# Optimization experiments

Measured on AMD Instinct MI355X. Metric: run time of the kernel, lower is better.

The kernel has to match this reference:

```python
import jax, jax.numpy as jnp
import numpy as np

# ---- model / batching constants (DeepSeek-LLM-7B attention, chunked prefill) ----
B = 8            # sequences in the continuous batch
Q_LEN = 512      # new (query) tokens per sequence
HIST = 512       # history tokens already in cache
NH = 32          # query heads
NKV = 32         # kv heads (== NH for deepseek 7B)
HD = 128         # head dim
HIDDEN = NH * HD # 4096
BS = 64          # paged-cache block size
NBLK = 16        # blocks per sequence -> kv_len = 1024
KV_LEN = BS * NBLK
NUM_BLOCKS = B * NBLK
ROPE_BASE = 10000.0


def rotate_half(x):
    x1, x2 = jnp.split(x, 2, axis=-1)
    return jnp.concatenate([-x2, x1], axis=-1)


def setup_inputs() -> dict:
    key = jax.random.key(0)
    ks = jax.random.split(key, 8)
    T = B * Q_LEN
    hidden_states = jax.random.normal(ks[0], (T, HIDDEN), jnp.float32)
    Wq = jax.random.normal(ks[1], (HIDDEN, NH * HD), jnp.float32) * 0.02
    Wk = jax.random.normal(ks[2], (HIDDEN, NKV * HD), jnp.float32) * 0.02
    Wv = jax.random.normal(ks[3], (HIDDEN, NKV * HD), jnp.float32) * 0.02
    Wo = jax.random.normal(ks[4], (NH * HD, HIDDEN), jnp.float32) * 0.02
    # paged KV cache; first HIST positions of each sequence hold history K/V
    k_cache = jax.random.normal(ks[5], (NUM_BLOCKS, BS, NKV, HD), jnp.float32) * 0.5
    v_cache = jax.random.normal(ks[6], (NUM_BLOCKS, BS, NKV, HD), jnp.float32) * 0.5
    # block table: each sequence gets NBLK distinct physical blocks (permuted)
    block_offsets = jnp.asarray(
        np.random.default_rng(0).permutation(NUM_BLOCKS).reshape(B, NBLK),
        jnp.int32)
    # per-token absolute position within its sequence (history offset + local idx)
    position_ids_1d = (jnp.arange(T, dtype=jnp.int32) % Q_LEN) + HIST
    kv_seq_length = jnp.full((B,), HIST + Q_LEN, jnp.int32)
    return dict(hidden_states=hidden_states, Wq=Wq, Wk=Wk, Wv=Wv, Wo=Wo,
                k_cache=k_cache, v_cache=v_cache, block_offsets=block_offsets,
                position_ids_1d=position_ids_1d, kv_seq_length=kv_seq_length)


def reference(hidden_states, Wq, Wk, Wv, Wo, k_cache, v_cache,
              block_offsets, position_ids_1d, kv_seq_length):
    T = hidden_states.shape[0]
    # --- QKV projections ---
    q = (hidden_states @ Wq).reshape(T, NH, HD)
    k = (hidden_states @ Wk).reshape(T, NKV, HD)
    v = (hidden_states @ Wv).reshape(T, NKV, HD)
    # --- RoPE (per-token positions, continuous batching) ---
    inv_freq = 1.0 / (ROPE_BASE ** (jnp.arange(0, HD, 2, dtype=jnp.float32) / HD))
    freqs = position_ids_1d.astype(jnp.float32)[:, None] * inv_freq  # [T, HD/2]
    emb = jnp.concatenate([freqs, freqs], axis=-1)                    # [T, HD]
    cos = jnp.cos(emb)[:, None, :]
    sin = jnp.sin(emb)[:, None, :]
    q = q * cos + rotate_half(q) * sin
    k = k * cos + rotate_half(k) * sin
    # --- fill_kv_cache: scatter new K/V into paged cache via block table ---
    seq_idx = jnp.arange(T, dtype=jnp.int32) // Q_LEN
    blk = block_offsets[seq_idx, position_ids_1d // BS]  # [T] physical block id
    slot = position_ids_1d % BS                          # [T] slot within block
    k_cache = k_cache.at[blk, slot].set(k)
    v_cache = v_cache.at[blk, slot].set(v)
    # --- paged_attention_fwd: gather per-seq K/V via block table ---
    K = k_cache[block_offsets].reshape(B, KV_LEN, NKV, HD)
    V = v_cache[block_offsets].reshape(B, KV_LEN, NKV, HD)
    qb = q.reshape(B, Q_LEN, NH, HD)
    scale = 1.0 / jnp.sqrt(jnp.float32(HD))
    scores = jnp.einsum('bqhd,bkhd->bhqk', qb, K) * scale  # [B,NH,Q,KV]
    kv_pos = jnp.arange(KV_LEN, dtype=jnp.int32)
    q_pos = position_ids_1d.reshape(B, Q_LEN)
    mask = (kv_pos[None, None, :] <= q_pos[:, :, None]) & \
           (kv_pos[None, None, :] < kv_seq_length[:, None, None])  # [B,Q,KV]
    scores = jnp.where(mask[:, None, :, :], scores, jnp.finfo(scores.dtype).min)
    attn = jax.nn.softmax(scores, axis=-1)
    out = jnp.einsum('bhqk,bkhd->bqhd', attn, V).reshape(T, NH * HD)
    return out @ Wo
```

## Files before the change

kernel.cpp:

```cpp
#include <hip/hip_runtime.h>
#include <math.h>

typedef __bf16 bf16x8 __attribute__((ext_vector_type(8)));
typedef float floatx4 __attribute__((ext_vector_type(4)));
typedef unsigned short ushortx4 __attribute__((ext_vector_type(4)));
typedef unsigned short ushortx8 __attribute__((ext_vector_type(8)));

#define DEV __device__ __forceinline__

DEV unsigned short f2bf(float f){
  unsigned int u = __float_as_uint(f);
  return (unsigned short)((u + 0x7fffu + ((u >> 16) & 1u)) >> 16);
}
DEV float bf2f(unsigned short h){ return __uint_as_float(((unsigned int)h) << 16); }

DEV void gld16(const void* g, void* l){
  __builtin_amdgcn_global_load_lds((const __attribute__((address_space(1))) void*)g,
                                   (__attribute__((address_space(3))) void*)l, 16, 0, 0);
}
DEV floatx4 mfma16(bf16x8 a, bf16x8 b, floatx4 c){
  return __builtin_amdgcn_mfma_f32_16x16x32_bf16(a, b, c, 0, 0, 0);
}

#define NH 32
#define HD 128
#define QL 512
#define KVL 1024
#define HID 4096

__global__ void k_convert(const float* __restrict__ src, unsigned short* __restrict__ dst){
  size_t u = (size_t)blockIdx.x*256 + threadIdx.x;
  float4 a = ((const float4*)src)[2*u];
  float4 b = ((const float4*)src)[2*u+1];
  ushortx8 o;
  o[0]=f2bf(a.x); o[1]=f2bf(a.y); o[2]=f2bf(a.z); o[3]=f2bf(a.w);
  o[4]=f2bf(b.x); o[5]=f2bf(b.y); o[6]=f2bf(b.z); o[7]=f2bf(b.w);
  ((ushortx8*)dst)[u] = o;
}

__global__ void k_transpose_w(const float* __restrict__ W0, const float* __restrict__ W1,
                              const float* __restrict__ W2, const float* __restrict__ W3,
                              unsigned short* __restrict__ Wt){
  int bx = blockIdx.x, by = blockIdx.y, z = blockIdx.z;
  const float* src = (z==0)?W0:(z==1)?W1:(z==2)?W2:W3;
  __shared__ float t[64][65];
  int tid = threadIdx.x;
  int rr = tid >> 4, cc = tid & 15;
  #pragma unroll
  for (int p = 0; p < 4; ++p){
    int row = p*16 + rr;
    float4 v = *(const float4*)(src + (size_t)(by*64+row)*HID + bx*64 + cc*4);
    t[row][cc*4+0]=v.x; t[row][cc*4+1]=v.y; t[row][cc*4+2]=v.z; t[row][cc*4+3]=v.w;
  }
  __syncthreads();
  unsigned short* dst = Wt + (size_t)z*HID*HID;
  #pragma unroll
  for (int p = 0; p < 4; ++p){
    int orow = p*16 + rr;
    ushortx4 o;
    o[0]=f2bf(t[cc*4+0][orow]); o[1]=f2bf(t[cc*4+1][orow]);
    o[2]=f2bf(t[cc*4+2][orow]); o[3]=f2bf(t[cc*4+3][orow]);
    *(ushortx4*)(dst + (size_t)(bx*64+orow)*HID + by*64 + cc*4) = o;
  }
}

template<int MODE>
__global__ __launch_bounds__(256, 4) void k_gemm(
    const unsigned short* __restrict__ A, const unsigned short* __restrict__ Bt,
    float* __restrict__ Cf, unsigned short* __restrict__ Qr,
    unsigned short* __restrict__ Kf, unsigned short* __restrict__ Vtmp,
    int K, int N, int Ntiles)
{
  __shared__ __align__(16) unsigned short As[128*32];
  __shared__ __align__(16) unsigned short Bs[128*32];
  const int tid = threadIdx.x;
  const int wave = tid >> 6, lane = tid & 63;
  const int lm = lane & 15, quad = lane >> 4;
  const int wm = wave >> 1, wn = wave & 1;

  int lin = blockIdx.x;
  int xcd = lin & 7, loc = lin >> 3;
  int per = Ntiles * 2;
  int phase = loc / per, rr2 = loc - phase*per;
  const int bm = xcd*4 + phase*2 + (rr2 & 1);
  const int bn = rr2 >> 1;

  const char* gA[2]; const char* gB[2];
  unsigned short* lA[2]; unsigned short* lB[2];
  #pragma unroll
  for (int jj = 0; jj < 2; ++jj){
    int issue = wave*2 + jj;
    int row = issue*16 + (lane >> 2);
    int c = (lane & 3) ^ ((row >> 1) & 3);
    gA[jj] = (const char*)(A + (size_t)(bm*128 + row)*K) + c*16;
    gB[jj] = (const char*)(Bt + (size_t)(bn*128 + row)*K) + c*16;
    lA[jj] = As + issue*512;
    lB[jj] = Bs + issue*512;
  }
  floatx4 acc[4][4];
  #pragma unroll
  for (int i=0;i<4;i++)
    #pragma unroll
    for (int j=0;j<4;j++) acc[i][j] = (floatx4){0.f,0.f,0.f,0.f};

  int aoff[4], boff[4];
  #pragma unroll
  for (int i=0;i<4;i++){
    int rowA = wm*64 + i*16 + lm;
    aoff[i] = rowA*32 + (quad ^ ((rowA>>1)&3))*8;
    int rowB = wn*64 + i*16 + lm;
    boff[i] = rowB*32 + (quad ^ ((rowB>>1)&3))*8;
  }

  const int kIter = K >> 5;
  for (int kt = 0; kt < kIter; ++kt){
    #pragma unroll
    for (int jj=0;jj<2;jj++){ gld16(gA[jj], lA[jj]); gld16(gB[jj], lB[jj]); }
    __syncthreads();
    bf16x8 af[4], bfr[4];
    #pragma unroll
    for (int i=0;i<4;i++) af[i]  = *(const bf16x8*)(As + aoff[i]);
    #pragma unroll
    for (int i=0;i<4;i++) bfr[i] = *(const bf16x8*)(Bs + boff[i]);
    #pragma unroll
    for (int mi=0;mi<4;mi++)
      #pragma unroll
      for (int ni=0;ni<4;ni++)
        acc[mi][ni] = mfma16(af[mi], bfr[ni], acc[mi][ni]);
    __syncthreads();
    #pragma unroll
    for (int jj=0;jj<2;jj++){ gA[jj] += 64; gB[jj] += 64; }
  }

  #pragma unroll
  for (int mi=0;mi<4;mi++){
    #pragma unroll
    for (int ni=0;ni<4;ni++){
      #pragma unroll
      for (int r=0;r<4;r++){
        int trow = bm*128 + wm*64 + mi*16 + quad*4 + r;
        int col  = bn*128 + wn*64 + ni*16 + lm;
        float val = acc[mi][ni][r];
        if (MODE == 0){
          Cf[(size_t)trow*N + col] = val;
        } else {
          unsigned short bv = f2bf(val);
          int b = trow >> 9, qi = trow & 511;
          if (col < 4096){
            int hh = col >> 7, hd = col & 127;
            Qr[((size_t)(b*NH + hh)*QL + qi)*HD + hd] = bv;
          } else if (col < 8192){
            int cc2 = col - 4096; int hh = cc2 >> 7, hd = cc2 & 127;
            Kf[((size_t)(b*NH + hh)*KVL + 512 + qi)*HD + hd] = bv;
          } else {
            Vtmp[(size_t)trow*HID + (col - 8192)] = bv;
          }
        }
      }
    }
  }
}

__global__ void k_rope(unsigned short* __restrict__ Qr, unsigned short* __restrict__ Kf,
                       const int* __restrict__ pos_ids){
  int u = blockIdx.x*256 + threadIdx.x;
  int i = u & 63;
  int grp = u >> 6;
  int qi = grp & 511;
  int h = (grp >> 9) & 31;
  int b = grp >> 14;
  int t = b*QL + qi;
  int pos = pos_ids[t];
  float ang = (float)pos * exp2f((float)i * -0.20762050593046014f);
  float s, c;
  sincosf(ang, &s, &c);
  unsigned short* qp = Qr + ((size_t)(b*NH + h)*QL + qi)*HD;
  float x = bf2f(qp[i]), y = bf2f(qp[i+64]);
  qp[i]    = f2bf(x*c - y*s);
  qp[i+64] = f2bf(y*c + x*s);
  unsigned short* kp = Kf + ((size_t)(b*NH + h)*KVL + 512 + qi)*HD;
  x = bf2f(kp[i]); y = bf2f(kp[i+64]);
  kp[i]    = f2bf(x*c - y*s);
  kp[i+64] = f2bf(y*c + x*s);
}

__global__ void k_gather_k(const float* __restrict__ k_cache, const int* __restrict__ block_offsets,
                           unsigned short* __restrict__ Kf){
  int u = blockIdx.x*256 + threadIdx.x;
  int c4 = u & 31;
  int h  = (u >> 5) & 31;
  int kv = (u >> 10) & 511;
  int b  = u >> 19;
  int blk = block_offsets[b*16 + (kv >> 6)];
  int slot = kv & 63;
  float4 v = *(const float4*)(k_cache + ((size_t)(blk*64 + slot)*NH + h)*HD + c4*4);
  ushortx4 o; o[0]=f2bf(v.x); o[1]=f2bf(v.y); o[2]=f2bf(v.z); o[3]=f2bf(v.w);
  *(ushortx4*)(Kf + ((size_t)(b*NH + h)*KVL + kv)*HD + c4*4) = o;
}

__global__ void k_transpose_v(const float* __restrict__ v_cache, const unsigned short* __restrict__ Vtmp,
                              const int* __restrict__ block_offsets, unsigned short* __restrict__ Vt){
  int kvt = blockIdx.x, h = blockIdx.y, b = blockIdx.z;
  __shared__ __align__(16) unsigned short tt[64*132];
  int tid = threadIdx.x;
  #pragma unroll
  for (int p=0;p<8;p++){
    int cc = p*256 + tid;
    int slot = cc >> 5, c4 = cc & 31;
    ushortx4 val;
    if (kvt < 8){
      int blk = block_offsets[b*16 + kvt];
      float4 f = *(const float4*)(v_cache + ((size_t)(blk*64 + slot)*NH + h)*HD + c4*4);
      val[0]=f2bf(f.x); val[1]=f2bf(f.y); val[2]=f2bf(f.z); val[3]=f2bf(f.w);
    } else {
      val = *(const ushortx4*)(Vtmp + (size_t)(b*QL + (kvt-8)*64 + slot)*HID + h*HD + c4*4);
    }
    *(ushortx4*)(tt + slot*132 + c4*4) = val;
  }
  __syncthreads();
  #pragma unroll
  for (int p=0;p<8;p++){
    int cc = p*256 + tid;
    int hd = cc >> 4, s4 = cc & 15;
    ushortx4 o;
    o[0]=tt[(s4*4+0)*132 + hd];
    o[1]=tt[(s4*4+1)*132 + hd];
    o[2]=tt[(s4*4+2)*132 + hd];
    o[3]=tt[(s4*4+3)*132 + hd];
    *(ushortx4*)(Vt + ((size_t)(b*NH + h)*HD + hd)*KVL + kvt*64 + s4*4) = o;
  }
}

DEV void stage128(const char* srcBase, unsigned short* lds, int rowStrideBytes, int wave, int lane){
  #pragma unroll
  for (int jj=0;jj<8;jj++){
    int issue = wave*8 + jj;
    int row = issue*4 + (lane >> 4);
    int c = (lane & 15) ^ (row & 15);
    gld16(srcBase + (size_t)row*rowStrideBytes + c*16, lds + issue*512);
  }
}
DEV bf16x8 frag_swz(const unsigned short* lds, int row, int ks, int quad){
  int c = (ks*4 + quad) ^ (row & 15);
  return *(const bf16x8*)(lds + row*128 + c*8);
}

#define PSTR 144

__global__ __launch_bounds__(256, 1) void k_attn(
    const unsigned short* __restrict__ Qr, const unsigned short* __restrict__ Kf,
    const unsigned short* __restrict__ Vt, unsigned short* __restrict__ AO)
{
  int qt = blockIdx.x, h = blockIdx.y, b = blockIdx.z;
  int tid = threadIdx.x, wave = tid >> 6, lane = tid & 63;
  int lm = lane & 15, quad = lane >> 4;
  __shared__ __align__(16) unsigned short KS[2][128*128];
  __shared__ __align__(16) unsigned short VS[128*128];
  __shared__ __align__(16) unsigned short PS[4*32*PSTR];
  const char* Qbase = (const char*)(Qr + ((size_t)(b*NH + h)*QL + qt*128)*HD);
  const char* Kbase = (const char*)(Kf + ((size_t)(b*NH + h)*KVL)*HD);
  const char* Vbase = (const char*)(Vt + ((size_t)(b*NH + h)*HD)*KVL);

  stage128(Qbase, VS, 256, wave, lane);
  stage128(Kbase, KS[0], 256, wave, lane);
  __syncthreads();
  bf16x8 qf[2][4];
  #pragma unroll
  for (int mt=0;mt<2;mt++)
    #pragma unroll
    for (int ks=0;ks<4;ks++)
      qf[mt][ks] = frag_swz(VS, wave*32 + mt*16 + lm, ks, quad);
  __syncthreads();

  float m_st[2][4], l_st[2][4];
  floatx4 o[2][8];
  #pragma unroll
  for (int mt=0;mt<2;mt++){
    #pragma unroll
    for (int r=0;r<4;r++){ m_st[mt][r] = -3.0e38f; l_st[mt][r] = 0.f; }
    #pragma unroll
    for (int nt=0;nt<8;nt++) o[mt][nt] = (floatx4){0.f,0.f,0.f,0.f};
  }
  unsigned short* myP = PS + wave*(32*PSTR);
  const int sig = ((lm & 3) << 2) | (lm >> 2);
  const float scale = 0.08838834764831845f;
  int ntiles = qt + 5;

  for (int j=0;j<ntiles;j++){
    const unsigned short* cur = KS[j & 1];
    unsigned short* nxt = (unsigned short*)KS[(j+1) & 1];
    stage128(Vbase + (size_t)j*256, VS, 2048, wave, lane);
    if (j+1 < ntiles) stage128(Kbase + (size_t)(j+1)*128*256, nxt, 256, wave, lane);

    floatx4 s[2][8];
    #pragma unroll
    for (int nt=0;nt<8;nt++){
      bf16x8 kf4[4];
      #pragma unroll
      for (int ks=0;ks<4;ks++) kf4[ks] = frag_swz(cur, nt*16 + lm, ks, quad);
      #pragma unroll
      for (int mt=0;mt<2;mt++){
        floatx4 a = (floatx4){0.f,0.f,0.f,0.f};
        #pragma unroll
        for (int ks=0;ks<4;ks++) a = mfma16(qf[mt][ks], kf4[ks], a);
        s[mt][nt] = a;
      }
    }
    bool diag = (j == qt + 4);
    #pragma unroll
    for (int mt=0;mt<2;mt++){
      #pragma unroll
      for (int r=0;r<4;r++){
        int rowl = wave*32 + mt*16 + quad*4 + r;
        float mx = -3.0e38f;
        #pragma unroll
        for (int nt=0;nt<8;nt++){
          float v = s[mt][nt][r] * scale;
          if (diag && (nt*16 + lm > rowl)) v = -3.0e38f;
          s[mt][nt][r] = v;
          mx = fmaxf(mx, v);
        }
        mx = fmaxf(mx, __shfl_xor(mx, 1));
        mx = fmaxf(mx, __shfl_xor(mx, 2));
        mx = fmaxf(mx, __shfl_xor(mx, 4));
        mx = fmaxf(mx, __shfl_xor(mx, 8));
        float mold = m_st[mt][r];
        float mnew = fmaxf(mold, mx);
        float alpha = __expf(mold - mnew);
        m_st[mt][r] = mnew;
        float rs = 0.f;
        #pragma unroll
        for (int nt=0;nt<8;nt++){
          float p = __expf(s[mt][nt][r] - mnew);
          s[mt][nt][r] = p;
          rs += p;
        }
        rs += __shfl_xor(rs, 1);
        rs += __shfl_xor(rs, 2);
        rs += __shfl_xor(rs, 4);
        rs += __shfl_xor(rs, 8);
        l_st[mt][r] = l_st[mt][r]*alpha + rs;
        #pragma unroll
        for (int nt=0;nt<8;nt++) o[mt][nt][r] *= alpha;
      }
    }
    #pragma unroll
    for (int mt=0;mt<2;mt++)
      #pragma unroll
      for (int nt=0;nt<8;nt++)
        #pragma unroll
        for (int r=0;r<4;r++)
          myP[(mt*16 + r*4 + quad)*PSTR + nt*16 + lm] = f2bf(s[mt][nt][r]);

    __syncthreads();

    bf16x8 pf[2][4];
    #pragma unroll
    for (int mt=0;mt<2;mt++)
      #pragma unroll
      for (int ks=0;ks<4;ks++)
        pf[mt][ks] = *(const bf16x8*)(myP + (mt*16 + sig)*PSTR + ks*32 + quad*8);

    #pragma unroll
    for (int nt=0;nt<8;nt++){
      bf16x8 vf4[4];
      #pragma unroll
      for (int ks=0;ks<4;ks++) vf4[ks] = frag_swz(VS, nt*16 + lm, ks, quad);
      #pragma unroll
      for (int mt=0;mt<2;mt++){
        floatx4 a = o[mt][nt];
        #pragma unroll
        for (int ks=0;ks<4;ks++) a = mfma16(pf[mt][ks], vf4[ks], a);
        o[mt][nt] = a;
      }
    }
    __syncthreads();
  }

  #pragma unroll
  for (int mt=0;mt<2;mt++){
    #pragma unroll
    for (int r=0;r<4;r++){
      float inv = 1.f / l_st[mt][r];
      #pragma unroll
      for (int nt=0;nt<8;nt++){
        int trow = b*QL + qt*128 + wave*32 + mt*16 + quad*4 + r;
        int col = h*HD + nt*16 + lm;
        AO[(size_t)trow*HID + col] = f2bf(o[mt][nt][r] * inv);
      }
    }
  }
}

extern "C" void kernel_launch(void* const* d_in, const int* in_sizes, int n_in,
                              void* d_out, int out_size, void* d_ws, size_t ws_size,
                              hipStream_t stream) {
  const float* hidden   = (const float*)d_in[0];
  const float* Wq       = (const float*)d_in[1];
  const float* Wk       = (const float*)d_in[2];
  const float* Wv       = (const float*)d_in[3];
  const float* Wo       = (const float*)d_in[4];
  const float* k_cache  = (const float*)d_in[5];
  const float* v_cache  = (const float*)d_in[6];
  const int* block_offsets = (const int*)d_in[7];
  const int* pos_ids    = (const int*)d_in[8];
  float* out = (float*)d_out;

  char* ws = (char*)d_ws;
  unsigned short* hb   = (unsigned short*)(ws + 0x0);
  unsigned short* Wt   = (unsigned short*)(ws + 0x2000000);
  unsigned short* Qr   = (unsigned short*)(ws + 0xA000000);
  unsigned short* Kf   = (unsigned short*)(ws + 0xC000000);
  unsigned short* Vt   = (unsigned short*)(ws + 0x10000000);
  unsigned short* Vtmp = (unsigned short*)(ws + 0x14000000);
  unsigned short* AO   = hb;

  k_convert<<<8192, 256, 0, stream>>>(hidden, hb);
  k_transpose_w<<<dim3(64,64,4), 256, 0, stream>>>(Wq, Wk, Wv, Wo, Wt);
  k_gemm<1><<<3072, 256, 0, stream>>>(hb, Wt, nullptr, Qr, Kf, Vtmp, 4096, 12288, 96);
  k_rope<<<32768, 256, 0, stream>>>(Qr, Kf, pos_ids);
  k_gather_k<<<16384, 256, 0, stream>>>(k_cache, block_offsets, Kf);
  k_transpose_v<<<dim3(16,32,8), 256, 0, stream>>>(v_cache, Vtmp, block_offsets, Vt);
  k_attn<<<dim3(4,32,8), 256, 0, stream>>>(Qr, Kf, Vt, AO);
  k_gemm<0><<<1024, 256, 0, stream>>>(AO, Wt + (size_t)3*4096*4096, out,
                                      nullptr, nullptr, nullptr, 4096, 4096, 32);
}
```

Before: 1.368 ms.

## Rewrite GEMM as 256x256 tile, 8-wave, double-buffered LDS pipeline with staged prefetch

The bf16 MFMA GEMM used for the QKV and output projections moves from 128x128 tiles with 4 waves and a single LDS buffer (K step 32) to 256x256 tiles with 8 waves, K step 64 and double-buffered LDS. Global-to-LDS loads for the next one or two K steps are issued in quarters interleaved with the MFMA phases, using explicit vmcnt waits, barriers and setprio. This aims to hide memory latency and raise data reuse per loaded byte. In exchange it uses far more LDS and registers, launches fewer blocks (768 and 256), and relies on hand-tuned wait counts that are easy to get wrong.

```diff
diff --git a/kernel.cpp b/kernel.cpp
--- a/kernel.cpp
+++ b/kernel.cpp
@@ -64,82 +64,136 @@
   }
 }
 
-template<int MODE>
-__global__ __launch_bounds__(256, 4) void k_gemm(
+template<int MODE, int NTILES>
+__global__ __launch_bounds__(512, 2) void k_gemm(
     const unsigned short* __restrict__ A, const unsigned short* __restrict__ Bt,
     float* __restrict__ Cf, unsigned short* __restrict__ Qr,
     unsigned short* __restrict__ Kf, unsigned short* __restrict__ Vtmp,
-    int K, int N, int Ntiles)
+    int K, int N)
 {
-  __shared__ __align__(16) unsigned short As[128*32];
-  __shared__ __align__(16) unsigned short Bs[128*32];
+  __shared__ __align__(16) unsigned short As[2][256*64];
+  __shared__ __align__(16) unsigned short Bs[2][256*64];
   const int tid = threadIdx.x;
   const int wave = tid >> 6, lane = tid & 63;
   const int lm = lane & 15, quad = lane >> 4;
-  const int wm = wave >> 1, wn = wave & 1;
-
-  int lin = blockIdx.x;
-  int xcd = lin & 7, loc = lin >> 3;
-  int per = Ntiles * 2;
-  int phase = loc / per, rr2 = loc - phase*per;
-  const int bm = xcd*4 + phase*2 + (rr2 & 1);
-  const int bn = rr2 >> 1;
-
-  const char* gA[2]; const char* gB[2];
+  const int wm = wave >> 2, wn = wave & 3;
+
+  const int lin = blockIdx.x;
+  const int xcd = lin & 7, loc = lin >> 3;
+  const int bm = xcd*2 + loc / NTILES;
+  const int bn = loc % NTILES;
+  const int NT = K >> 6;
+
+  const unsigned short* gA[2]; const unsigned short* gB[2];
   unsigned short* lA[2]; unsigned short* lB[2];
   #pragma unroll
-  for (int jj = 0; jj < 2; ++jj){
-    int issue = wave*2 + jj;
-    int row = issue*16 + (lane >> 2);
-    int c = (lane & 3) ^ ((row >> 1) & 3);
-    gA[jj] = (const char*)(A + (size_t)(bm*128 + row)*K) + c*16;
-    gB[jj] = (const char*)(Bt + (size_t)(bn*128 + row)*K) + c*16;
-    lA[jj] = As + issue*512;
-    lB[jj] = Bs + issue*512;
-  }
-  floatx4 acc[4][4];
-  #pragma unroll
-  for (int i=0;i<4;i++)
+  for (int j=0;j<2;j++){
+    int rh = (wave*2 + j)*8 + (lane >> 3);
+    int cswz = ((lane & 7) ^ (rh & 7)) * 8;
+    gA[j] = A  + (size_t)(bm*256 + rh)*K + cswz;
+    gB[j] = Bt + (size_t)(bn*256 + rh)*K + cswz;
+    lA[j] = &As[0][0] + (wave*2 + j)*512;
+    lB[j] = &Bs[0][0] + (wave*2 + j)*512;
+  }
+  auto STAGE = [&](int u, int kind){
+    const int bo  = (u & 1) * 16384 + (kind & 1) * 8192;
+    const size_t go = (size_t)(kind & 1) * 128 * (size_t)K + (size_t)u * 64;
+    if (kind < 2){
+      #pragma unroll
+      for (int j=0;j<2;j++) gld16(gB[j] + go, lB[j] + bo);
+    } else {
+      #pragma unroll
+      for (int j=0;j<2;j++) gld16(gA[j] + go, lA[j] + bo);
+    }
+  };
+
+  const int rbA = (wm*128 + lm)*64;
+  const int rbB = (wn*64  + lm)*64;
+  const int cx0 = ( quad      ^ (lm & 7))*8;
+  const int cx1 = ((4 + quad) ^ (lm & 7))*8;
+
+  floatx4 acc[8][4];
+  #pragma unroll
+  for (int i=0;i<8;i++)
     #pragma unroll
     for (int j=0;j<4;j++) acc[i][j] = (floatx4){0.f,0.f,0.f,0.f};
 
-  int aoff[4], boff[4];
-  #pragma unroll
-  for (int i=0;i<4;i++){
-    int rowA = wm*64 + i*16 + lm;
-    aoff[i] = rowA*32 + (quad ^ ((rowA>>1)&3))*8;
-    int rowB = wn*64 + i*16 + lm;
-    boff[i] = rowB*32 + (quad ^ ((rowB>>1)&3))*8;
-  }
-
-  const int kIter = K >> 5;
-  for (int kt = 0; kt < kIter; ++kt){
-    #pragma unroll
-    for (int jj=0;jj<2;jj++){ gld16(gA[jj], lA[jj]); gld16(gB[jj], lB[jj]); }
-    __syncthreads();
-    bf16x8 af[4], bfr[4];
-    #pragma unroll
-    for (int i=0;i<4;i++) af[i]  = *(const bf16x8*)(As + aoff[i]);
-    #pragma unroll
-    for (int i=0;i<4;i++) bfr[i] = *(const bf16x8*)(Bs + boff[i]);
-    #pragma unroll
-    for (int mi=0;mi<4;mi++)
-      #pragma unroll
-      for (int ni=0;ni<4;ni++)
-        acc[mi][ni] = mfma16(af[mi], bfr[ni], acc[mi][ni]);
-    __syncthreads();
-    #pragma unroll
-    for (int jj=0;jj<2;jj++){ gA[jj] += 64; gB[jj] += 64; }
-  }
-
-  #pragma unroll
-  for (int mi=0;mi<4;mi++){
+  STAGE(0,0); STAGE(0,1); STAGE(0,2); STAGE(0,3);
+  asm volatile("s_waitcnt vmcnt(4)" ::: "memory");
+  STAGE(1,0); STAGE(1,1); STAGE(1,2);
+  asm volatile("s_waitcnt vmcnt(6)" ::: "memory");
+  __builtin_amdgcn_sched_barrier(0);
+  __builtin_amdgcn_s_barrier();
+  __builtin_amdgcn_sched_barrier(0);
+
+  bf16x8 afr[8][2], bfr[4][2];
+
+  for (int t = 0; t < NT; ++t){
+    const unsigned short* Ab = &As[t&1][0];
+    const unsigned short* Bb = &Bs[t&1][0];
+    #pragma unroll
+    for (int p = 0; p < 4; ++p){
+      if (p == 0){
+        #pragma unroll
+        for (int n=0;n<4;n++){
+          bfr[n][0] = *(const bf16x8*)(Bb + rbB + n*1024 + cx0);
+          bfr[n][1] = *(const bf16x8*)(Bb + rbB + n*1024 + cx1);
+        }
+        #pragma unroll
+        for (int m=0;m<2;m++){
+          afr[m][0] = *(const bf16x8*)(Ab + rbA + m*1024 + cx0);
+          afr[m][1] = *(const bf16x8*)(Ab + rbA + m*1024 + cx1);
+        }
+        if (t+1 < NT) STAGE(t+1, 3);
+      } else if (p == 1){
+        #pragma unroll
+        for (int m=2;m<4;m++){
+          afr[m][0] = *(const bf16x8*)(Ab + rbA + m*1024 + cx0);
+          afr[m][1] = *(const bf16x8*)(Ab + rbA + m*1024 + cx1);
+        }
+        if (t+2 < NT) STAGE(t+2, 0);
+      } else if (p == 2){
+        #pragma unroll
+        for (int m=4;m<8;m++){
+          afr[m][0] = *(const bf16x8*)(Ab + rbA + m*1024 + cx0);
+          afr[m][1] = *(const bf16x8*)(Ab + rbA + m*1024 + cx1);
+        }
+        if (t+2 < NT) STAGE(t+2, 1);
+      } else {
+        if (t+2 < NT) STAGE(t+2, 2);
+      }
+      __builtin_amdgcn_sched_barrier(0);
+      __builtin_amdgcn_s_barrier();
+      __builtin_amdgcn_sched_barrier(0);
+      __builtin_amdgcn_s_setprio(1);
+      #pragma unroll
+      for (int mm = 2*p; mm < 2*p + 2; ++mm)
+        #pragma unroll
+        for (int n = 0; n < 4; ++n){
+          floatx4 a = acc[mm][n];
+          a = mfma16(afr[mm][0], bfr[n][0], a);
+          a = mfma16(afr[mm][1], bfr[n][1], a);
+          acc[mm][n] = a;
+        }
+      __builtin_amdgcn_s_setprio(0);
+      if (p == 3){
+        if (t < NT-2)       asm volatile("s_waitcnt vmcnt(6)" ::: "memory");
+        else if (t == NT-2) asm volatile("s_waitcnt vmcnt(0)" ::: "memory");
+      }
+      __builtin_amdgcn_sched_barrier(0);
+      __builtin_amdgcn_s_barrier();
+      __builtin_amdgcn_sched_barrier(0);
+    }
+  }
+
+  #pragma unroll
+  for (int mi=0;mi<8;mi++){
     #pragma unroll
     for (int ni=0;ni<4;ni++){
       #pragma unroll
       for (int r=0;r<4;r++){
-        int trow = bm*128 + wm*64 + mi*16 + quad*4 + r;
-        int col  = bn*128 + wn*64 + ni*16 + lm;
+        int trow = bm*256 + wm*128 + mi*16 + quad*4 + r;
+        int col  = bn*256 + wn*64  + ni*16 + lm;
         float val = acc[mi][ni][r];
         if (MODE == 0){
           Cf[(size_t)trow*N + col] = val;
@@ -417,11 +471,11 @@
 
   k_convert<<<8192, 256, 0, stream>>>(hidden, hb);
   k_transpose_w<<<dim3(64,64,4), 256, 0, stream>>>(Wq, Wk, Wv, Wo, Wt);
-  k_gemm<1><<<3072, 256, 0, stream>>>(hb, Wt, nullptr, Qr, Kf, Vtmp, 4096, 12288, 96);
+  k_gemm<1,48><<<768, 512, 0, stream>>>(hb, Wt, nullptr, Qr, Kf, Vtmp, 4096, 12288);
   k_rope<<<32768, 256, 0, stream>>>(Qr, Kf, pos_ids);
   k_gather_k<<<16384, 256, 0, stream>>>(k_cache, block_offsets, Kf);
   k_transpose_v<<<dim3(16,32,8), 256, 0, stream>>>(v_cache, Vtmp, block_offsets, Vt);
   k_attn<<<dim3(4,32,8), 256, 0, stream>>>(Qr, Kf, Vt, AO);
-  k_gemm<0><<<1024, 256, 0, stream>>>(AO, Wt + (size_t)3*4096*4096, out,
-                                      nullptr, nullptr, nullptr, 4096, 4096, 32);
-}
+  k_gemm<0,16><<<256, 512, 0, stream>>>(AO, Wt + (size_t)3*4096*4096, out,
+                                        nullptr, nullptr, nullptr, 4096, 4096);
+}
```

Measured after the change: 1.281 ms. 1.07x faster.
